# Performance work log

Hardware: AMD Instinct MI355X
Metric: run time of the kernel (lower is better)

The kernel has to match this reference:

```python
import jax, jax.numpy as jnp
import numpy as np

B, C, H, W = 4, 64, 256, 256
WIDE = 256      # num_features * width_multiplier
K = 4           # dynamic kernel banks
KS = 3          # kernel size
RED = 16        # channels // reduction = 64 // 4
PAD = KS // 2


def _wn(v, g):
    # torch weight_norm, dim=0: norm over all dims except leading dim
    n = jnp.sqrt(jnp.sum(v * v, axis=tuple(range(1, v.ndim)), keepdims=True))
    return g * v / n


def _conv(x, w, groups=1):
    return jax.lax.conv_general_dilated(
        x, w, window_strides=(1, 1), padding=[(PAD, PAD), (PAD, PAD)],
        feature_group_count=groups, dimension_numbers=('NCHW', 'OIHW', 'NCHW'))


def setup_inputs() -> dict:
    key = jax.random.key(0)
    ks = jax.random.split(key, 16)
    s = lambda k, shape, sc: jax.random.normal(k, shape, jnp.float32) * sc
    return {
        'x': jax.random.normal(ks[0], (B, C, H, W), jnp.float32),
        'scale': jax.random.uniform(ks[1], (B, 1), jnp.float32, 1.0, 4.0),
        # body conv 1 (weight-normed, ReLU)
        'v1': s(ks[2], (WIDE, C, KS, KS), 0.05), 'g1': jnp.ones((WIDE, 1, 1, 1), jnp.float32),
        'b1': jnp.zeros((WIDE,), jnp.float32),
        # body conv 2 (weight-normed, no act)
        'v2': s(ks[3], (C, WIDE, KS, KS), 0.05), 'g2': jnp.ones((C, 1, 1, 1), jnp.float32),
        'b2': jnp.zeros((C,), jnp.float32),
        # scale-aware dynamic conv: K banks of [C_out, C_in, k, k], weight-normed over dim 0 (=K)
        'dyn_v': s(ks[4], (K, C, C, KS, KS), 0.05), 'dyn_g': jnp.ones((K, 1, 1, 1, 1), jnp.float32),
        'dyn_b': jnp.zeros((K, C), jnp.float32),
        # routing: Linear(1 -> K) + softmax
        'att_w': s(ks[5], (1, K), 1.0), 'att_b': jnp.zeros((K,), jnp.float32),
        # SE block: Linear(C -> C/red, no bias), ReLU, Linear(C/red -> C, no bias), Sigmoid
        'se_w1': s(ks[6], (RED, C), 0.1), 'se_w2': s(ks[7], (C, RED), 0.1),
    }


def reference(x, scale, v1, g1, b1, v2, g2, b2, dyn_v, dyn_g, dyn_b,
              att_w, att_b, se_w1, se_w2):
    # --- body: wide weight-normed conv stack ---
    r = jax.nn.relu(_conv(x, _wn(v1, g1)) + b1[None, :, None, None])   # [B,WIDE,H,W]
    r = _conv(r, _wn(v2, g2)) + b2[None, :, None, None]                # [B,C,H,W]
    # --- scale-aware dynamic conv: per-sample softmax mix of K kernels ---
    att = jax.nn.softmax(scale @ att_w + att_b, axis=-1)               # [B,K]
    w_bank = _wn(dyn_v, dyn_g)                                         # [K,C,C,k,k]
    w_b = jnp.einsum('bk,koicd->boicd', att, w_bank)                   # [B,C,C,k,k]
    bias_b = att @ dyn_b                                               # [B,C]
    # batch-grouped conv: one distinct kernel per sample
    y = _conv(r.reshape(1, B * C, H, W), w_b.reshape(B * C, C, KS, KS), groups=B)
    y = y.reshape(B, C, H, W) + bias_b[:, :, None, None]
    # --- SE gating ---
    p = jnp.mean(y, axis=(2, 3))                                       # [B,C]
    gate = jax.nn.sigmoid(jax.nn.relu(p @ se_w1.T) @ se_w2.T)          # [B,C]
    y = y * gate[:, :, None, None]
    # --- residual ---
    return x + y
```

## Files before the change

### kernel.cpp

```cpp
#include <hip/hip_runtime.h>

typedef __attribute__((ext_vector_type(8))) short short8;
typedef __attribute__((ext_vector_type(4))) float f32x4;

#define HH 256
#define WW 256

static constexpr size_t PS_IN = (size_t)4 * HH * WW * 32;

__device__ inline unsigned int f2bf(float x) {
  unsigned int u = __float_as_uint(x);
  return (u + 0x7fffu + ((u >> 16) & 1u)) >> 16;
}
__device__ inline unsigned int pack2(float a, float b) {
  return f2bf(a) | (f2bf(b) << 16);
}

__global__ __launch_bounds__(256) void xpose_k(const float* __restrict__ x,
                                               unsigned short* __restrict__ xcl) {
  const int t = threadIdx.x;
  const int ci = t & 63;
  const int wv = t >> 6;
  const int x0 = blockIdx.x * 64;
  const int y  = blockIdx.y;
  const int b  = blockIdx.z;
  const float* src = x + ((size_t)(b * 64 + ci) * HH + y) * WW + x0 + wv;
  unsigned short* dst = xcl + (size_t)(ci >> 5) * PS_IN +
                        ((size_t)((b * HH + y) * WW) + x0 + wv) * 32 + (ci & 31);
#pragma unroll
  for (int k = 0; k < 16; ++k)
    dst[(size_t)k * 4 * 32] = (unsigned short)f2bf(src[4 * k]);
}

template <int COUT, int CINK>
__global__ __launch_bounds__(256) void wnorm_k(const float* __restrict__ v,
                                               const float* __restrict__ g,
                                               unsigned short* __restrict__ out) {
  constexpr int N = CINK * 9;
  constexpr size_t APS = (size_t)9 * COUT * 32;
  const int co = blockIdx.x, t = threadIdx.x;
  const float* vb = v + (size_t)co * N;
  float s = 0.f;
  for (int i = t; i < N; i += 256) { float a = vb[i]; s += a * a; }
  for (int off = 32; off > 0; off >>= 1) s += __shfl_xor(s, off, 64);
  __shared__ float red[4];
  if ((t & 63) == 0) red[t >> 6] = s;
  __syncthreads();
  const float tot = red[0] + red[1] + red[2] + red[3];
  const float sc = g[co] / sqrtf(tot);
  for (int i = t; i < N; i += 256) {
    int ci = i / 9, tap = i - 9 * (i / 9);
    out[(size_t)(ci >> 5) * APS + ((size_t)tap * COUT + co) * 32 + (ci & 31)] =
        (unsigned short)f2bf(vb[i] * sc);
  }
}

__global__ __launch_bounds__(256) void dynnorm_k(const float* __restrict__ dyn_v,
                                                 const float* __restrict__ dyn_g,
                                                 float* __restrict__ dscale) {
  const int k = blockIdx.x, t = threadIdx.x;
  const float* vb = dyn_v + (size_t)k * 36864;
  float s = 0.f;
  for (int i = t; i < 36864; i += 256) { float a = vb[i]; s += a * a; }
  for (int off = 32; off > 0; off >>= 1) s += __shfl_xor(s, off, 64);
  __shared__ float red[4];
  if ((t & 63) == 0) red[t >> 6] = s;
  __syncthreads();
  if (t == 0) dscale[k] = dyn_g[k] / sqrtf(red[0] + red[1] + red[2] + red[3]);
}

__global__ __launch_bounds__(256) void mix_k(const float* __restrict__ scale,
                                             const float* __restrict__ att_w,
                                             const float* __restrict__ att_b,
                                             const float* __restrict__ dyn_v,
                                             const float* __restrict__ dyn_b,
                                             const float* __restrict__ dscale,
                                             unsigned short* __restrict__ wbt,
                                             float* __restrict__ bias_b,
                                             float* __restrict__ zp) {
  const int blk = blockIdx.x;
  const int b = blk >> 6, co = blk & 63;
  const int t = threadIdx.x;
  float att[4], wsc[4];
  const float sc = scale[b];
  float mx = -1e30f;
#pragma unroll
  for (int k = 0; k < 4; ++k) { att[k] = sc * att_w[k] + att_b[k]; mx = fmaxf(mx, att[k]); }
  float den = 0.f;
#pragma unroll
  for (int k = 0; k < 4; ++k) { att[k] = expf(att[k] - mx); den += att[k]; }
#pragma unroll
  for (int k = 0; k < 4; ++k) { att[k] /= den; wsc[k] = att[k] * dscale[k]; }
  for (int i = t; i < 576; i += 256) {
    int ci = i / 9, tap = i - 9 * (i / 9);
    float w = 0.f;
#pragma unroll
    for (int k = 0; k < 4; ++k)
      w += wsc[k] * dyn_v[(((size_t)k * 64 + co) * 64 + ci) * 9 + tap];
    wbt[(size_t)b * 36864 + (size_t)(ci >> 5) * 18432 + ((size_t)tap * 64 + co) * 32 + (ci & 31)] =
        (unsigned short)f2bf(w);
  }
  if (t == 0) {
    float bb = 0.f;
#pragma unroll
    for (int k = 0; k < 4; ++k) bb += att[k] * dyn_b[k * 64 + co];
    bias_b[blk] = bb;
  }
  if (blk == 0) zp[t] = 0.f;
}

template <int CIN, int COUT, bool RELU, bool DYN>
__global__ __launch_bounds__(512, 2) void conv3x3_mfma(const unsigned short* __restrict__ in_cl,
                                                       const unsigned short* __restrict__ wt,
                                                       const float* __restrict__ bias,
                                                       unsigned short* __restrict__ out_cl,
                                                       float* __restrict__ y_out,
                                                       float* __restrict__ pblk,
                                                       const float* __restrict__ zp) {
  constexpr int CO_TILES = COUT / 64;
  constexpr int NCH = CIN / 32;
  constexpr int NSLOT = 2448;
  constexpr size_t APS = (size_t)9 * COUT * 32;
  const int tid = threadIdx.x;
  const int lane = tid & 63;
  const int wv = tid >> 6;
  const int l15 = lane & 15;
  const int lg = lane >> 4;

  const int wg = (blockIdx.x & 7) * (gridDim.x >> 3) + (blockIdx.x >> 3);
  int tdec = wg;
  const int cot = tdec % CO_TILES; tdec /= CO_TILES;
  const int bx = tdec & 7; tdec >>= 3;
  const int by = tdec & 15; tdec >>= 4;
  const int bz = tdec;

  const int x0 = bx * 32;
  const int y0 = by * 16;
  const int co0 = cot * 64;

  const unsigned short* inb = in_cl + (size_t)bz * HH * WW * 32;
  const unsigned short* wtb = wt + (DYN ? (size_t)bz * NCH * APS : (size_t)0);
  const float* biasb = bias + (DYN ? bz * 64 : 0);
  const unsigned short* zp16 = (const unsigned short*)zp;

  __shared__ __align__(16) char lds[131072];

  const unsigned short* sptr[5];
  size_t istep[5];
#pragma unroll
  for (int k = 0; k < 5; ++k) {
    const int u = k * 512 + tid;
    const int pair = u >> 3;
    const int s = ((u & 7) * 16) ^ ((pair & 7) << 4);
    const int parity = s >> 6;
    const int g = (s >> 4) & 3;
    const int px = 2 * pair + parity;
    const int row = px / 34, col = px - 34 * row;
    const int gy = y0 - 1 + row, gx = x0 - 1 + col;
    const bool ok = (u < NSLOT) && ((unsigned)gy < (unsigned)HH) && ((unsigned)gx < (unsigned)WW);
    sptr[k] = ok ? (inb + ((size_t)(gy * WW + gx)) * 32 + g * 8) : zp16;
    istep[k] = ok ? PS_IN : 0;
  }
  int dyA[2], gA[2], coA[2];
  bool aval[2];
#pragma unroll
  for (int r = 0; r < 2; ++r) {
    const int slot = r * 512 + tid;
    dyA[r] = slot >> 8;
    gA[r] = (slot >> 6) & 3;
    coA[r] = slot & 63;
    aval[r] = (slot < 768);
  }

  f32x4 acc[4][4];
#pragma unroll
  for (int m = 0; m < 4; ++m)
#pragma unroll
    for (int n = 0; n < 4; ++n) acc[m][n] = (f32x4){0.f, 0.f, 0.f, 0.f};

#define STAGE_I(c, IBOFS)                                                          \
  do {                                                                             \
    _Pragma("unroll") for (int k_ = 0; k_ < 5; ++k_)                               \
        __builtin_amdgcn_global_load_lds(                                          \
            (const void*)(sptr[k_] + (size_t)(c) * istep[k_]),                     \
            (void*)(lds + (IBOFS) + (k_ * 512 + wv * 64) * 16), 16, 0, 0);         \
  } while (0)

#define STAGE_A(d, c, bidx)                                                        \
  do {                                                                             \
    _Pragma("unroll") for (int r_ = 0; r_ < 2; ++r_) {                             \
      const unsigned short* s_ =                                                   \
          aval[r_] ? wt_base + (size_t)(c) * APS +                                 \
                         ((size_t)((dyA[r_] * 3 + (d)) * COUT + co0 + coA[r_])) * 32 + \
                         gA[r_] * 8                                                \
                   : zp16;                                                         \
      __builtin_amdgcn_global_load_lds(                                            \
          (const void*)s_,                                                         \
          (void*)(lds + 81920 + (bidx) * 16384 + (r_ * 512 + wv * 64) * 16), 16, 0, 0); \
    }                                                                              \
  } while (0)

#define PHASE(DXV, IBOFS, WAITN, ...)                                              \
  do {                                                                             \
    short8 Af[3][4], Bv[2][4];                                                     \
    {                                                                              \
      const char* aB_ = lds + 81920 + (DXV) * 16384;                               \
      _Pragma("unroll") for (int dy = 0; dy < 3; ++dy)                             \
          _Pragma("unroll") for (int m = 0; m < 4; ++m)                            \
              Af[dy][m] = *(const short8*)(aB_ + (dy * 4 + lg) * 1024 +            \
                                           (16 * m + l15) * 16);                   \
      const char* iB_ = lds + (IBOFS);                                             \
      _Pragma("unroll") for (int c2 = 0; c2 < 2; ++c2)                             \
          _Pragma("unroll") for (int bi = 0; bi < 4; ++bi) {                       \
        const int px_ = (2 * wv + bi) * 34 + 16 * c2 + l15 + (DXV);                \
        const int by_ = (px_ >> 1) * 128 +                                         \
                        ((lg * 16 + (px_ & 1) * 64) ^ (((px_ >> 1) & 7) << 4));    \
        Bv[c2][bi] = *(const short8*)(iB_ + by_);                                  \
      }                                                                            \
    }                                                                              \
    __VA_ARGS__;                                                                   \
    __builtin_amdgcn_s_setprio(1);                                                 \
    _Pragma("unroll") for (int c2 = 0; c2 < 2; ++c2)                               \
        _Pragma("unroll") for (int bi = 0; bi < 4; ++bi)                           \
            _Pragma("unroll") for (int dy = 0; dy < 3; ++dy) {                     \
      if (dy < ((bi > 1) ? (bi - 1) : 0) || dy > ((bi < 2) ? bi : 2)) continue;    \
      const int n_ = 2 * (bi - dy) + c2;                                           \
      _Pragma("unroll") for (int m = 0; m < 4; ++m)                                \
          acc[m][n_] = __builtin_amdgcn_mfma_f32_16x16x32_bf16(Af[dy][m],          \
                                                               Bv[c2][bi],        \
                                                               acc[m][n_], 0, 0, 0); \
    }                                                                              \
    __builtin_amdgcn_s_setprio(0);                                                 \
    asm volatile("s_waitcnt vmcnt(" #WAITN ")" ::: "memory");                      \
    __builtin_amdgcn_s_barrier();                                                  \
  } while (0)

  const unsigned short* wt_base = wtb;

  STAGE_I(0, 0);
  STAGE_A(0, 0, 0);
  STAGE_A(1, 0, 1);
  asm volatile("s_waitcnt vmcnt(2)" ::: "memory");
  __builtin_amdgcn_s_barrier();

#pragma unroll 1
  for (int ch = 0; ch < NCH - 1; ++ch) {
    const int ib = (ch & 1) * 40960;
    const int ibn = 40960 - ib;
    PHASE(0, ib, 7, STAGE_A(2, ch, 2); STAGE_I(ch + 1, ibn));
    PHASE(1, ib, 7, STAGE_A(0, ch + 1, 0));
    PHASE(2, ib, 2, STAGE_A(1, ch + 1, 1));
  }
  {
    const int ib = ((NCH - 1) & 1) * 40960;
    PHASE(0, ib, 2, STAGE_A(2, NCH - 1, 2));
    PHASE(1, ib, 0, (void)0);
    PHASE(2, ib, 0, (void)0);
  }
#undef PHASE
#undef STAGE_A
#undef STAGE_I

  float scol[4][4];
  if (DYN) {
#pragma unroll
    for (int m = 0; m < 4; ++m)
#pragma unroll
      for (int f = 0; f < 4; ++f) scol[m][f] = 0.f;
  }

#pragma unroll
  for (int m = 0; m < 4; ++m) {
    const f32x4 bs = *(const f32x4*)(biasb + co0 + 16 * m + 4 * lg);
#pragma unroll
    for (int n = 0; n < 4; ++n) {
      f32x4 v = acc[m][n] + bs;
      if (RELU) {
        v.x = fmaxf(v.x, 0.f); v.y = fmaxf(v.y, 0.f);
        v.z = fmaxf(v.z, 0.f); v.w = fmaxf(v.w, 0.f);
      }
      const int yy = y0 + 2 * wv + (n >> 1);
      const int xx = x0 + 16 * (n & 1) + l15;
      if (!DYN) {
        uint2 pk;
        pk.x = pack2(v.x, v.y);
        pk.y = pack2(v.z, v.w);
        const int co = co0 + 16 * m + 4 * lg;
        *(uint2*)(out_cl + (size_t)(co >> 5) * PS_IN +
                  ((size_t)((bz * HH + yy) * WW + xx)) * 32 + (co & 31)) = pk;
      } else {
        const size_t base = ((size_t)(bz * 64 + 16 * m + 4 * lg) * HH + yy) * WW + xx;
        y_out[base]             = v.x;
        y_out[base + 1 * 65536] = v.y;
        y_out[base + 2 * 65536] = v.z;
        y_out[base + 3 * 65536] = v.w;
        scol[m][0] += v.x; scol[m][1] += v.y; scol[m][2] += v.z; scol[m][3] += v.w;
      }
    }
  }
  if (DYN) {
#pragma unroll
    for (int m = 0; m < 4; ++m)
#pragma unroll
      for (int f = 0; f < 4; ++f) {
        float r = scol[m][f];
        r += __shfl_xor(r, 1, 64);
        r += __shfl_xor(r, 2, 64);
        r += __shfl_xor(r, 4, 64);
        r += __shfl_xor(r, 8, 64);
        scol[m][f] = r;
      }
    __syncthreads();
    float* red = (float*)lds;
    if (l15 == 0) {
#pragma unroll
      for (int m = 0; m < 4; ++m)
#pragma unroll
        for (int f = 0; f < 4; ++f)
          red[wv * 64 + 16 * m + 4 * lg + f] = scol[m][f];
    }
    __syncthreads();
    if (tid < 64) {
      float s = 0.f;
#pragma unroll
      for (int w = 0; w < 8; ++w) s += red[w * 64 + tid];
      pblk[((size_t)bz * 128 + by * 8 + bx) * 64 + tid] = s;
    }
  }
}

__global__ __launch_bounds__(256) void gate_k(const float* __restrict__ pblk,
                                              const float* __restrict__ se_w1,
                                              const float* __restrict__ se_w2,
                                              float* __restrict__ gate) {
  const int b = blockIdx.x;
  const int t = threadIdx.x;
  const int c = t & 63, part = t >> 6;
  __shared__ float ps[4][64];
  __shared__ float p_s[64], h_s[16];
  float s = 0.f;
  for (int blk = part; blk < 128; blk += 4)
    s += pblk[((size_t)b * 128 + blk) * 64 + c];
  ps[part][c] = s;
  __syncthreads();
  if (t < 64) p_s[t] = (ps[0][t] + ps[1][t] + ps[2][t] + ps[3][t]) * (1.f / 65536.f);
  __syncthreads();
  if (t < 16) {
    float h = 0.f;
    for (int cc = 0; cc < 64; ++cc) h += p_s[cc] * se_w1[t * 64 + cc];
    h_s[t] = fmaxf(h, 0.f);
  }
  __syncthreads();
  if (t < 64) {
    float a = 0.f;
    for (int j = 0; j < 16; ++j) a += h_s[j] * se_w2[t * 16 + j];
    gate[b * 64 + t] = 1.f / (1.f + expf(-a));
  }
}

__global__ __launch_bounds__(256) void final_k(const float* __restrict__ x,
                                               const float* __restrict__ gate,
                                               float* __restrict__ out) {
  const size_t i = ((size_t)blockIdx.x * 256 + threadIdx.x) * 4;
  f32x4 yv = *(f32x4*)(out + i);
  const f32x4 xv = *(const f32x4*)(x + i);
  const float g = gate[(int)(i >> 16)];
  yv = xv + yv * g;
  *(f32x4*)(out + i) = yv;
}

static constexpr size_t SZ_XCL = (size_t)4 * 256 * 256 * 64 * 2;
static constexpr size_t SZ_W   = (size_t)9 * 256 * 64 * 2;
static constexpr size_t SZ_PBLK = (size_t)4 * 128 * 64 * 4;

static constexpr size_t B_XCL = 0;
static constexpr size_t B_R   = B_XCL + SZ_XCL;
static constexpr size_t B_W1T = B_R + 4 * SZ_XCL;
static constexpr size_t B_W2T = B_W1T + SZ_W;
static constexpr size_t B_WBT = B_W2T + SZ_W;
static constexpr size_t B_DSC = B_WBT + SZ_W;
static constexpr size_t B_BB  = B_DSC + 256;
static constexpr size_t B_GT  = B_BB + 1024;
static constexpr size_t B_ZP  = B_GT + 1024;
static constexpr size_t B_PBLK = B_ZP + 1024;
static constexpr size_t WS_BIG = B_PBLK + SZ_PBLK;

extern "C" void kernel_launch(void* const* d_in, const int* in_sizes, int n_in,
                              void* d_out, int out_size, void* d_ws, size_t ws_size,
                              hipStream_t stream) {
  (void)in_sizes; (void)n_in; (void)out_size;
  if (ws_size < WS_BIG) return;

  const float* x     = (const float*)d_in[0];
  const float* scale = (const float*)d_in[1];
  const float* v1    = (const float*)d_in[2];
  const float* g1    = (const float*)d_in[3];
  const float* b1    = (const float*)d_in[4];
  const float* v2    = (const float*)d_in[5];
  const float* g2    = (const float*)d_in[6];
  const float* b2    = (const float*)d_in[7];
  const float* dyn_v = (const float*)d_in[8];
  const float* dyn_g = (const float*)d_in[9];
  const float* dyn_b = (const float*)d_in[10];
  const float* att_w = (const float*)d_in[11];
  const float* att_b = (const float*)d_in[12];
  const float* se_w1 = (const float*)d_in[13];
  const float* se_w2 = (const float*)d_in[14];
  float* out = (float*)d_out;

  char* ws = (char*)d_ws;
  unsigned short* xcl  = (unsigned short*)(ws + B_XCL);
  unsigned short* rbuf = (unsigned short*)(ws + B_R);
  unsigned short* r2   = (unsigned short*)(ws + B_XCL);
  unsigned short* w1t  = (unsigned short*)(ws + B_W1T);
  unsigned short* w2t  = (unsigned short*)(ws + B_W2T);
  unsigned short* wbt  = (unsigned short*)(ws + B_WBT);
  float* dscale = (float*)(ws + B_DSC);
  float* bias_b = (float*)(ws + B_BB);
  float* gate   = (float*)(ws + B_GT);
  float* zp     = (float*)(ws + B_ZP);
  float* pblk   = (float*)(ws + B_PBLK);

  xpose_k<<<dim3(4, 256, 4), 256, 0, stream>>>(x, xcl);
  wnorm_k<256, 64><<<256, 256, 0, stream>>>(v1, g1, w1t);
  wnorm_k<64, 256><<<64, 256, 0, stream>>>(v2, g2, w2t);
  dynnorm_k<<<4, 256, 0, stream>>>(dyn_v, dyn_g, dscale);
  mix_k<<<256, 256, 0, stream>>>(scale, att_w, att_b, dyn_v, dyn_b, dscale, wbt, bias_b, zp);

  conv3x3_mfma<64, 256, true, false><<<2048, 512, 0, stream>>>(
      xcl, w1t, b1, rbuf, nullptr, nullptr, zp);
  conv3x3_mfma<256, 64, false, false><<<512, 512, 0, stream>>>(
      rbuf, w2t, b2, r2, nullptr, nullptr, zp);
  conv3x3_mfma<64, 64, false, true><<<512, 512, 0, stream>>>(
      r2, wbt, bias_b, nullptr, out, pblk, zp);

  gate_k<<<4, 256, 0, stream>>>(pblk, se_w1, se_w2, gate);
  final_k<<<16384, 256, 0, stream>>>(x, gate, out);
}
```

Baseline: 327.2 us.

## Single-buffer input tile via register staging to shrink LDS footprint

Drops the double-buffered input halo tile in LDS. The next chunk's input is now loaded into registers during phase 0 and written to LDS after phase 2, behind an extra barrier. Weight buffers are packed tighter and unused weight-slot loads are redirected to a dummy LDS slot, which cuts LDS use from 128KB to 76KB so that two workgroups may fit per CU. The cost is extra VGPRs for the staged input, an additional barrier and LDS write per chunk, and less overlap of input loads with compute.

Result: slower. 389.9 us (+19.2%).

```diff
diff --git a/kernel.cpp b/kernel.cpp
--- a/kernel.cpp
+++ b/kernel.cpp
@@ -139,11 +139,11 @@
   const int co0 = cot * 64;
 
   const unsigned short* inb = in_cl + (size_t)bz * HH * WW * 32;
-  const unsigned short* wtb = wt + (DYN ? (size_t)bz * NCH * APS : (size_t)0);
+  const unsigned short* wt_base = wt + (DYN ? (size_t)bz * NCH * APS : (size_t)0);
   const float* biasb = bias + (DYN ? bz * 64 : 0);
   const unsigned short* zp16 = (const unsigned short*)zp;
 
-  __shared__ __align__(16) char lds[131072];
+  __shared__ __align__(16) char lds[77824];
 
   const unsigned short* sptr[5];
   size_t istep[5];
@@ -162,14 +162,14 @@
     istep[k] = ok ? PS_IN : 0;
   }
   int dyA[2], gA[2], coA[2];
-  bool aval[2];
+  bool awv[2];
 #pragma unroll
   for (int r = 0; r < 2; ++r) {
     const int slot = r * 512 + tid;
     dyA[r] = slot >> 8;
     gA[r] = (slot >> 6) & 3;
     coA[r] = slot & 63;
-    aval[r] = (slot < 768);
+    awv[r] = (r * 512 + wv * 64) < 768;
   }
 
   f32x4 acc[4][4];
@@ -177,45 +177,36 @@
   for (int m = 0; m < 4; ++m)
 #pragma unroll
     for (int n = 0; n < 4; ++n) acc[m][n] = (f32x4){0.f, 0.f, 0.f, 0.f};
-
-#define STAGE_I(c, IBOFS)                                                          \
-  do {                                                                             \
-    _Pragma("unroll") for (int k_ = 0; k_ < 5; ++k_)                               \
-        __builtin_amdgcn_global_load_lds(                                          \
-            (const void*)(sptr[k_] + (size_t)(c) * istep[k_]),                     \
-            (void*)(lds + (IBOFS) + (k_ * 512 + wv * 64) * 16), 16, 0, 0);         \
-  } while (0)
 
 #define STAGE_A(d, c, bidx)                                                        \
   do {                                                                             \
     _Pragma("unroll") for (int r_ = 0; r_ < 2; ++r_) {                             \
       const unsigned short* s_ =                                                   \
-          aval[r_] ? wt_base + (size_t)(c) * APS +                                 \
-                         ((size_t)((dyA[r_] * 3 + (d)) * COUT + co0 + coA[r_])) * 32 + \
-                         gA[r_] * 8                                                \
-                   : zp16;                                                         \
-      __builtin_amdgcn_global_load_lds(                                            \
-          (const void*)s_,                                                         \
-          (void*)(lds + 81920 + (bidx) * 16384 + (r_ * 512 + wv * 64) * 16), 16, 0, 0); \
+          awv[r_] ? wt_base + (size_t)(c) * APS +                                  \
+                        ((size_t)((dyA[r_] * 3 + (d)) * COUT + co0 + coA[r_])) * 32 + \
+                        gA[r_] * 8                                                 \
+                  : zp16;                                                          \
+      char* d_ = awv[r_] ? lds + 40960 + (bidx) * 12288 + (r_ * 512 + wv * 64) * 16 \
+                         : lds + 39936;                                            \
+      __builtin_amdgcn_global_load_lds((const void*)s_, (void*)d_, 16, 0, 0);      \
     }                                                                              \
   } while (0)
 
-#define PHASE(DXV, IBOFS, WAITN, ...)                                              \
+#define PHASE(DXV, WAITN, ...)                                                     \
   do {                                                                             \
     short8 Af[3][4], Bv[2][4];                                                     \
     {                                                                              \
-      const char* aB_ = lds + 81920 + (DXV) * 16384;                               \
+      const char* aB_ = lds + 40960 + (DXV) * 12288;                               \
       _Pragma("unroll") for (int dy = 0; dy < 3; ++dy)                             \
           _Pragma("unroll") for (int m = 0; m < 4; ++m)                            \
               Af[dy][m] = *(const short8*)(aB_ + (dy * 4 + lg) * 1024 +            \
                                            (16 * m + l15) * 16);                   \
-      const char* iB_ = lds + (IBOFS);                                             \
       _Pragma("unroll") for (int c2 = 0; c2 < 2; ++c2)                             \
           _Pragma("unroll") for (int bi = 0; bi < 4; ++bi) {                       \
         const int px_ = (2 * wv + bi) * 34 + 16 * c2 + l15 + (DXV);                \
         const int by_ = (px_ >> 1) * 128 +                                         \
                         ((lg * 16 + (px_ & 1) * 64) ^ (((px_ >> 1) & 7) << 4));    \
-        Bv[c2][bi] = *(const short8*)(iB_ + by_);                                  \
+        Bv[c2][bi] = *(const short8*)(lds + by_);                                  \
       }                                                                            \
     }                                                                              \
     __VA_ARGS__;                                                                   \
@@ -233,33 +224,41 @@
     __builtin_amdgcn_s_setprio(0);                                                 \
     asm volatile("s_waitcnt vmcnt(" #WAITN ")" ::: "memory");                      \
     __builtin_amdgcn_s_barrier();                                                  \
+    __builtin_amdgcn_sched_barrier(0);                                             \
   } while (0)
 
-  const unsigned short* wt_base = wtb;
-
-  STAGE_I(0, 0);
+#pragma unroll
+  for (int k = 0; k < 5; ++k)
+    __builtin_amdgcn_global_load_lds((const void*)sptr[k],
+                                     (void*)(lds + (k * 512 + wv * 64) * 16), 16, 0, 0);
   STAGE_A(0, 0, 0);
   STAGE_A(1, 0, 1);
-  asm volatile("s_waitcnt vmcnt(2)" ::: "memory");
+  asm volatile("s_waitcnt vmcnt(0)" ::: "memory");
   __builtin_amdgcn_s_barrier();
+  __builtin_amdgcn_sched_barrier(0);
 
 #pragma unroll 1
   for (int ch = 0; ch < NCH - 1; ++ch) {
-    const int ib = (ch & 1) * 40960;
-    const int ibn = 40960 - ib;
-    PHASE(0, ib, 7, STAGE_A(2, ch, 2); STAGE_I(ch + 1, ibn));
-    PHASE(1, ib, 7, STAGE_A(0, ch + 1, 0));
-    PHASE(2, ib, 2, STAGE_A(1, ch + 1, 1));
+    uint4 ireg[5];
+    PHASE(0, 7, STAGE_A(2, ch, 2);
+          _Pragma("unroll") for (int k_ = 0; k_ < 5; ++k_)
+              ireg[k_] = *(const uint4*)(sptr[k_] + (size_t)(ch + 1) * istep[k_]););
+    PHASE(1, 2, STAGE_A(0, ch + 1, 0));
+    PHASE(2, 2, STAGE_A(1, ch + 1, 1));
+#pragma unroll
+    for (int k = 0; k < 5; ++k)
+      *(uint4*)(lds + (size_t)(k * 512 + tid) * 16) = ireg[k];
+    asm volatile("s_waitcnt lgkmcnt(0)" ::: "memory");
+    __builtin_amdgcn_s_barrier();
+    __builtin_amdgcn_sched_barrier(0);
   }
   {
-    const int ib = ((NCH - 1) & 1) * 40960;
-    PHASE(0, ib, 2, STAGE_A(2, NCH - 1, 2));
-    PHASE(1, ib, 0, (void)0);
-    PHASE(2, ib, 0, (void)0);
+    PHASE(0, 2, STAGE_A(2, NCH - 1, 2));
+    PHASE(1, 0, (void)0);
+    PHASE(2, 0, (void)0);
   }
 #undef PHASE
 #undef STAGE_A
-#undef STAGE_I
 
   float scol[4][4];
   if (DYN) {
```
